# Performance work log

Measured on AMD Instinct MI355X. Metric: run time of the kernel, lower is better.

Reference implementation:

```python
import jax, jax.numpy as jnp
import numpy as np

N, E, H, K = 2000, 512, 8, 32
DH = E // H  # 64
CLAMP = 10000.0
LN_EPS = 1e-5


def _layernorm(x, g, b):
    mu = jnp.mean(x, axis=-1, keepdims=True)
    var = jnp.mean((x - mu) ** 2, axis=-1, keepdims=True)
    return (x - mu) * jax.lax.rsqrt(var + LN_EPS) * g + b


def setup_inputs() -> dict:
    key = jax.random.key(0)
    ks = jax.random.split(key, 16)
    s_in = 1.0 / np.sqrt(E)
    inp = {
        'x': jax.random.normal(ks[0], (N, E), jnp.float32),
        'coords9': jax.random.normal(ks[1], (N, 9), jnp.float32),
        'prompt_signal': jax.random.normal(ks[2], (E,), jnp.float32),
        # pos_encoder: Linear(3, E//4) + GELU + LayerNorm(E//4)
        'pos_w1': jax.random.normal(ks[3], (E // 4, 3), jnp.float32) * 0.5,
        'pos_b1': jax.random.normal(ks[4], (E // 4,), jnp.float32) * 0.02,
        'pos_ln_g': jnp.ones((E // 4,), jnp.float32),
        'pos_ln_b': jnp.zeros((E // 4,), jnp.float32),
        # MultiheadAttention in/out projections
        'wq': jax.random.normal(ks[5], (E, E), jnp.float32) * s_in,
        'wk': jax.random.normal(ks[6], (E, E), jnp.float32) * s_in,
        'wv': jax.random.normal(ks[7], (E, E), jnp.float32) * s_in,
        'bq': jnp.zeros((E,), jnp.float32),
        'bk': jnp.zeros((E,), jnp.float32),
        'bv': jnp.zeros((E,), jnp.float32),
        'wo': jax.random.normal(ks[8], (E, E), jnp.float32) * s_in,
        'bo': jnp.zeros((E,), jnp.float32),
    }
    return inp


def reference(x, coords9, prompt_signal, pos_w1, pos_b1, pos_ln_g, pos_ln_b,
              wq, wk, wv, bq, bk, bv, wo, bo):
    n = x.shape[0]
    # centroids of triangle faces: (N,3)
    centroids = coords9.reshape(n, 3, 3).mean(axis=1)
    # pairwise centroid distances (only relation feature that affects output)
    diff = centroids[:, None, :] - centroids[None, :, :]        # (N,N,3)
    distances = jnp.linalg.norm(diff, axis=-1)                   # (N,N)
    # positional encoding branch
    pos_enc = _layernorm(jax.nn.gelu(centroids @ pos_w1.T + pos_b1, approximate=False),
                         pos_ln_g, pos_ln_b)                     # (N,E/4)
    prompt_enhanced = x + prompt_signal[None, :]
    pos_enhanced = jnp.concatenate([prompt_enhanced[:, :3 * E // 4], pos_enc], axis=-1)  # (N,E)
    # top-k nearest neighbors mask (k smallest distances per row)
    _, topk_idx = jax.lax.top_k(-distances, K)                   # (N,K)
    attn_mask = jnp.full((n, n), -jnp.inf, jnp.float32)
    attn_mask = attn_mask.at[jnp.arange(n)[:, None], topk_idx].set(0.0)
    # multi-head attention, self q=k=v, fp32
    q = (pos_enhanced @ wq.T + bq).reshape(n, H, DH)
    k = (pos_enhanced @ wk.T + bk).reshape(n, H, DH)
    v = (pos_enhanced @ wv.T + bv).reshape(n, H, DH)
    scores = jnp.einsum('nhd,mhd->hnm', q, k) / np.sqrt(DH) + attn_mask[None]
    attn = jax.nn.softmax(scores, axis=-1)                       # (H,N,N)
    ctx = jnp.einsum('hnm,mhd->nhd', attn, v).reshape(n, E)
    out = ctx @ wo.T + bo
    # _sanitize_tensor
    out = jnp.nan_to_num(out, nan=0.0, posinf=CLAMP, neginf=-CLAMP)
    return jnp.clip(out, -CLAMP, CLAMP)
```

## Files before the change

kernel.cpp:

```cpp
#include <hip/hip_runtime.h>
#include <math.h>

#define NN_K 32
#define E_DIM 512
#define CLAMP_V 10000.0f

typedef __attribute__((ext_vector_type(8))) short short8;
typedef __attribute__((ext_vector_type(4))) float f32x4;

__device__ __forceinline__ unsigned short f2bf(float x) {
  unsigned u = __float_as_uint(x);
  unsigned r = u + 0x7fffu + ((u >> 16) & 1u);
  return (unsigned short)(r >> 16);
}
__device__ __forceinline__ float bf2f_bits(short h) {
  return __uint_as_float(((unsigned)(unsigned short)h) << 16);
}

__device__ __forceinline__ void async16(const void* g, void* l) {
  __builtin_amdgcn_global_load_lds((const __attribute__((address_space(1))) void*)g,
                                   (__attribute__((address_space(3))) void*)l, 16, 0, 0);
}

__global__ __launch_bounds__(256) void wconv_kernel(
    const float* __restrict__ wq, const float* __restrict__ wk,
    const float* __restrict__ wv, const float* __restrict__ wo,
    short* __restrict__ w_bf)
{
  int v = blockIdx.x * 256 + threadIdx.x;
  int m = v >> 16;
  int e = v & 0xffff;
  const float* src = m == 0 ? wq : (m == 1 ? wk : (m == 2 ? wv : wo));
  float4 f = ((const float4*)src)[e];
  short4 h;
  h.x = (short)f2bf(f.x); h.y = (short)f2bf(f.y);
  h.z = (short)f2bf(f.z); h.w = (short)f2bf(f.w);
  ((short4*)w_bf)[v] = h;
}

__global__ __launch_bounds__(128) void pos_kernel(
    const float* __restrict__ x, const float* __restrict__ coords9,
    const float* __restrict__ prompt,
    const float* __restrict__ w1, const float* __restrict__ b1,
    const float* __restrict__ ln_g, const float* __restrict__ ln_b,
    short* __restrict__ pos_bf, float* __restrict__ cent, int N)
{
  int n = blockIdx.x;
  int t = threadIdx.x;
  size_t rb = (size_t)n * E_DIM;
  if (n >= N) {
    #pragma unroll
    for (int j = t; j < E_DIM; j += 128) pos_bf[rb + j] = 0;
    return;
  }
  const float* c9 = coords9 + n * 9;
  float c0 = (c9[0] + c9[3] + c9[6]) / 3.0f;
  float c1 = (c9[1] + c9[4] + c9[7]) / 3.0f;
  float c2 = (c9[2] + c9[5] + c9[8]) / 3.0f;
  if (t == 0) { cent[n*3+0] = c0; cent[n*3+1] = c1; cent[n*3+2] = c2; }

  float pre = c0 * w1[t*3+0] + c1 * w1[t*3+1] + c2 * w1[t*3+2] + b1[t];
  float g = 0.5f * pre * (1.0f + erff(pre * 0.70710678118654752440f));

  __shared__ float red[4];
  float s = g;
  #pragma unroll
  for (int o = 32; o > 0; o >>= 1) s += __shfl_xor(s, o);
  if ((t & 63) == 0) red[t >> 6] = s;
  __syncthreads();
  float mu = (red[0] + red[1]) * (1.0f / 128.0f);
  float d = g - mu;
  float s2 = d * d;
  #pragma unroll
  for (int o = 32; o > 0; o >>= 1) s2 += __shfl_xor(s2, o);
  if ((t & 63) == 0) red[2 + (t >> 6)] = s2;
  __syncthreads();
  float var = (red[2] + red[3]) * (1.0f / 128.0f);
  float y = d * rsqrtf(var + 1e-5f) * ln_g[t] + ln_b[t];

  pos_bf[rb + 384 + t] = (short)f2bf(y);
  #pragma unroll
  for (int j = t; j < 384; j += 128)
    pos_bf[rb + j] = (short)f2bf(x[rb + j] + prompt[j]);
}

__global__ __launch_bounds__(256) void topk_kernel(
    const float* __restrict__ cent, int* __restrict__ topk, int N)
{
  __shared__ unsigned hist[256];
  __shared__ unsigned waveSums[4];
  __shared__ unsigned sel_bin, sel_rem;
  __shared__ unsigned cnt, tcnt;
  __shared__ unsigned tie[2048];

  int n = blockIdx.x;
  int t = threadIdx.x;
  int lane = t & 63, wid = t >> 6;
  float cx = cent[n*3+0], cy = cent[n*3+1], cz = cent[n*3+2];

  unsigned bits[8];
  #pragma unroll
  for (int r = 0; r < 8; ++r) {
    int m = t + (r << 8);
    unsigned b = 0xFFFFFFFFu;
    if (m < N) {
      float dx = cx - cent[m*3+0];
      float dy = cy - cent[m*3+1];
      float dz = cz - cent[m*3+2];
      float dist = sqrtf(dx*dx + dy*dy + dz*dz);
      b = __float_as_uint(dist);
    }
    bits[r] = b;
  }

  unsigned prefix = 0;
  unsigned K_rem = NN_K;
  #pragma unroll
  for (int p = 0; p < 4; ++p) {
    int shift = 24 - 8 * p;
    unsigned high_mask = (p == 0) ? 0u : (0xFFFFFFFFu << (8 * (4 - p)));
    hist[t] = 0;
    __syncthreads();
    #pragma unroll
    for (int r = 0; r < 8; ++r) {
      if ((bits[r] & high_mask) == prefix)
        atomicAdd(&hist[(bits[r] >> shift) & 255], 1u);
    }
    __syncthreads();
    unsigned h = hist[t];
    unsigned scan = h;
    #pragma unroll
    for (int o = 1; o < 64; o <<= 1) {
      unsigned u = __shfl_up(scan, o);
      if (lane >= o) scan += u;
    }
    if (lane == 63) waveSums[wid] = scan;
    __syncthreads();
    unsigned off = 0;
    for (int w = 0; w < wid; ++w) off += waveSums[w];
    scan += off;
    if (scan >= K_rem && (scan - h) < K_rem) {
      sel_bin = (unsigned)t;
      sel_rem = K_rem - (scan - h);
    }
    __syncthreads();
    prefix |= sel_bin << shift;
    K_rem = sel_rem;
    __syncthreads();
  }

  unsigned T = prefix;
  if (t == 0) { cnt = 0; tcnt = 0; }
  __syncthreads();
  #pragma unroll
  for (int r = 0; r < 8; ++r) {
    int m = t + (r << 8);
    if (m < N) {
      if (bits[r] < T) {
        unsigned slot = atomicAdd(&cnt, 1u);
        topk[n * NN_K + slot] = m;
      } else if (bits[r] == T) {
        unsigned tp = atomicAdd(&tcnt, 1u);
        tie[tp] = (unsigned)m;
      }
    }
  }
  __syncthreads();
  if (t == 0) {
    unsigned base = cnt;
    unsigned need = K_rem;
    for (unsigned it = 0; it < need; ++it) {
      unsigned best = 0xFFFFFFFFu, bj = 0;
      for (unsigned j = 0; j < tcnt; ++j)
        if (tie[j] < best) { best = tie[j]; bj = j; }
      topk[n * NN_K + base + it] = (int)best;
      tie[bj] = 0xFFFFFFFFu;
    }
  }
}

__device__ __forceinline__ void gemm_core(
    const short* __restrict__ A, const short* __restrict__ W,
    const float* __restrict__ bias,
    float* __restrict__ outf, short* __restrict__ outb,
    int out_ld, int out_c0,
    int M, int row0, int col0, bool doClamp)
{
  __shared__ short sA[2][4096], sB[2][4096];
  int tid = threadIdx.x;
  int cr = tid >> 2;
  int ck = (tid & 3) << 3;
  const short* gA = A + (size_t)(row0 + cr) * 512 + ck;
  const short* gB = W + (size_t)(col0 + cr) * 512 + ck;
  int lo0 = tid * 8, lo1 = (tid + 256) * 8;
  const size_t rstep = (size_t)64 * 512;

  int lane = tid & 63, wv_ = tid >> 6;
  int wm = (wv_ & 1) << 6, wn = (wv_ >> 1) << 6;
  int lr = lane & 15, lq = lane >> 4;

#define STAGE(t, b) do { \
    async16(gA + (t) * 32,         &sA[b][lo0]); \
    async16(gA + (t) * 32 + rstep, &sA[b][lo1]); \
    async16(gB + (t) * 32,         &sB[b][lo0]); \
    async16(gB + (t) * 32 + rstep, &sB[b][lo1]); } while (0)

  STAGE(0, 0);
  STAGE(1, 1);

  f32x4 acc[4][4];
  #pragma unroll
  for (int i = 0; i < 4; ++i)
    #pragma unroll
    for (int j = 0; j < 4; ++j)
      acc[i][j] = (f32x4){0.f, 0.f, 0.f, 0.f};

  #pragma unroll
  for (int it = 0; it < 16; ++it) {
    int cur = it & 1;
    if (it == 15) asm volatile("s_waitcnt vmcnt(0)\ns_barrier" ::: "memory");
    else          asm volatile("s_waitcnt vmcnt(4)\ns_barrier" ::: "memory");

    short8 af[4], bf[4];
    #pragma unroll
    for (int i = 0; i < 4; ++i) {
      af[i] = *(const short8*)&sA[cur][(wm + (i << 4) + lr) * 32 + (lq << 3)];
      bf[i] = *(const short8*)&sB[cur][(wn + (i << 4) + lr) * 32 + (lq << 3)];
    }
    #pragma unroll
    for (int i = 0; i < 4; ++i)
      #pragma unroll
      for (int j = 0; j < 4; ++j)
        acc[i][j] = __builtin_amdgcn_mfma_f32_16x16x32_bf16(af[i], bf[j], acc[i][j], 0, 0, 0);

    asm volatile("s_waitcnt lgkmcnt(0)\ns_barrier" ::: "memory");
    if (it + 2 < 16) STAGE(it + 2, cur);
  }
#undef STAGE

  #pragma unroll
  for (int j = 0; j < 4; ++j) {
    int gcol = col0 + wn + (j << 4) + lr;
    float bv_ = bias[gcol];
    #pragma unroll
    for (int i = 0; i < 4; ++i) {
      #pragma unroll
      for (int r = 0; r < 4; ++r) {
        int grow = row0 + wm + (i << 4) + (lq << 2) + r;
        if (grow < M) {
          float v = acc[i][j][r] + bv_;
          if (doClamp) {
            v = isnan(v) ? 0.0f : v;
            v = fminf(fmaxf(v, -CLAMP_V), CLAMP_V);
          }
          if (outf) outf[(size_t)grow * 512 + gcol] = v;
          else      outb[(size_t)grow * out_ld + out_c0 + gcol] = (short)f2bf(v);
        }
      }
    }
  }
}

__global__ __launch_bounds__(256) void qkv_mfma(
    const short* __restrict__ A, const short* __restrict__ Wb,
    const float* __restrict__ bq, const float* __restrict__ bk, const float* __restrict__ bv,
    float* __restrict__ qb, short* __restrict__ kv, int M)
{
  int sel = blockIdx.y >> 2;
  int nblk = blockIdx.y & 3;
  int r0 = blockIdx.x * 128, c0 = nblk * 128;
  if (sel == 0)
    gemm_core(A, Wb, bq, qb, nullptr, 512, 0, M, r0, c0, false);
  else if (sel == 1)
    gemm_core(A, Wb + 262144, bk, nullptr, kv, 1024, 0, M, r0, c0, false);
  else
    gemm_core(A, Wb + 2 * 262144, bv, nullptr, kv, 1024, 512, M, r0, c0, false);
}

__global__ __launch_bounds__(256) void out_mfma(
    const short* __restrict__ A, const short* __restrict__ Wb,
    const float* __restrict__ bias, float* __restrict__ out, int M)
{
  gemm_core(A, Wb + (size_t)3 * 262144, bias, out, nullptr, 512, 0, M,
            blockIdx.x * 128, blockIdx.y * 128, true);
}

__global__ __launch_bounds__(512) void attn_kernel(
    const float* __restrict__ qb, const short* __restrict__ kv,
    const int* __restrict__ topk, short* __restrict__ ctx_bf, int N)
{
  __shared__ short klds[32 * 512];
  __shared__ int sidx[NN_K];
  __shared__ float plds[8 * 32];

  int n = blockIdx.x;
  int tid = threadIdx.x;
  size_t rb = (size_t)n * E_DIM;
  if (n >= N) { ctx_bf[rb + tid] = 0; return; }

  if (tid < NN_K) sidx[tid] = topk[n * NN_K + tid];
  __syncthreads();

  int h = tid >> 6, lane = tid & 63;
  int jk = lane & 31, half = lane >> 5;
  int dbase = h * 64 + half * 32;

  float qv[32];
  {
    const float4* qs = (const float4*)(qb + rb + dbase);
    #pragma unroll
    for (int b = 0; b < 8; ++b) {
      float4 f = qs[b];
      qv[b*4+0] = f.x; qv[b*4+1] = f.y; qv[b*4+2] = f.z; qv[b*4+3] = f.w;
    }
  }

  {
    int j = tid >> 4, a = tid & 15;
    const short8* src = (const short8*)(kv + (size_t)sidx[j] * 1024 + a * 32);
    int sw = 4 * (j & 15);
    short* row = &klds[j * 512];
    #pragma unroll
    for (int b = 0; b < 4; ++b) {
      short8 val = src[b];
      int d0 = a * 32 + b * 8;
      *(short4*)&row[(d0    ) ^ sw] = *(const short4*)&val;
      *(short4*)&row[(d0 + 4) ^ sw] = *((const short4*)&val + 1);
    }
  }
  __syncthreads();

  float s = 0.f;
  {
    int sw = 4 * (jk & 15);
    const short* krow = &klds[jk * 512];
    #pragma unroll
    for (int i = 0; i < 32; ++i) {
      int d = (dbase + i) ^ sw;
      s += qv[i] * bf2f_bits(krow[d]);
    }
  }
  s += __shfl_xor(s, 32);
  s *= 0.125f;

  float mx = s;
  #pragma unroll
  for (int o = 16; o > 0; o >>= 1) mx = fmaxf(mx, __shfl_xor(mx, o));
  float p = expf(s - mx);
  float l = p;
  #pragma unroll
  for (int o = 16; o > 0; o >>= 1) l += __shfl_xor(l, o);
  p *= (1.0f / l);
  if (half == 0) plds[h * 32 + jk] = p;
  __syncthreads();

  float pv[32];
  #pragma unroll
  for (int b = 0; b < 8; ++b) {
    float4 f = *(const float4*)&plds[h * 32 + b * 4];
    pv[b*4+0] = f.x; pv[b*4+1] = f.y; pv[b*4+2] = f.z; pv[b*4+3] = f.w;
  }

  int off = 512 + h * 64 + lane;
  float acc = 0.f;
  #pragma unroll
  for (int j = 0; j < NN_K; ++j) {
    int ij = topk[n * NN_K + j];
    acc += pv[j] * bf2f_bits(kv[(size_t)ij * 1024 + off]);
  }
  ctx_bf[rb + h * 64 + lane] = (short)f2bf(acc);
}

extern "C" void kernel_launch(void* const* d_in, const int* in_sizes, int n_in,
                              void* d_out, int out_size, void* d_ws, size_t ws_size,
                              hipStream_t stream) {
  const float* x       = (const float*)d_in[0];
  const float* coords9 = (const float*)d_in[1];
  const float* prompt  = (const float*)d_in[2];
  const float* pos_w1  = (const float*)d_in[3];
  const float* pos_b1  = (const float*)d_in[4];
  const float* ln_g    = (const float*)d_in[5];
  const float* ln_b    = (const float*)d_in[6];
  const float* wq      = (const float*)d_in[7];
  const float* wk      = (const float*)d_in[8];
  const float* wv      = (const float*)d_in[9];
  const float* bq      = (const float*)d_in[10];
  const float* bk      = (const float*)d_in[11];
  const float* bv      = (const float*)d_in[12];
  const float* wo      = (const float*)d_in[13];
  const float* bo      = (const float*)d_in[14];

  int N = in_sizes[1] / 9;
  int Mpad = (N + 127) & ~127;
  size_t PE = (size_t)Mpad * E_DIM;

  char* p = (char*)d_ws;
  short* pos_bf = (short*)p; p += PE * 2;
  short* w_bf   = (short*)p; p += (size_t)4 * 512 * 512 * 2;
  float* qb     = (float*)p; p += PE * 4;
  short* kv_bf  = (short*)p; p += PE * 2 * 2;
  short* ctx_bf = (short*)p; p += PE * 2;
  float* cent   = (float*)p; p += (size_t)N * 3 * 4;
  int*   topk   = (int*)p;

  wconv_kernel<<<1024, 256, 0, stream>>>(wq, wk, wv, wo, w_bf);
  pos_kernel<<<Mpad, 128, 0, stream>>>(x, coords9, prompt, pos_w1, pos_b1,
                                       ln_g, ln_b, pos_bf, cent, N);
  topk_kernel<<<N, 256, 0, stream>>>(cent, topk, N);

  dim3 gq(Mpad / 128, 12);
  qkv_mfma<<<gq, 256, 0, stream>>>(pos_bf, w_bf, bq, bk, bv, qb, kv_bf, Mpad);
  attn_kernel<<<Mpad, 512, 0, stream>>>(qb, kv_bf, topk, ctx_bf, N);

  dim3 go(Mpad / 128, 4);
  out_mfma<<<go, 256, 0, stream>>>(ctx_bf, w_bf, bo, (float*)d_out, N);
}
```

Baseline: 168.0 us.

## Fuse weight conversion, pos-encoding and top-k into one kernel; shrink GEMM tiles

Merges the weight bf16 conversion, positional-encoding and top-k kernels into a single front kernel, dispatched by block index, to remove two launches and the centroid buffer. Centroids are now recomputed from coords9 inside the top-k path. The shared GEMM core moves from 128x128 to 64x128 tiles so the QKV and output projections launch twice as many blocks, which should fill more CUs but lowers per-block reuse. The attention kernel also reads K rows with short4 loads and takes neighbour indices from shared memory instead of reloading them from global memory. The front kernel's branch boundary is hardcoded to 2304 blocks, which only matches Mpad = 2048.

```diff
diff --git a/kernel.cpp b/kernel.cpp
--- a/kernel.cpp
+++ b/kernel.cpp
@@ -22,159 +22,172 @@
                                    (__attribute__((address_space(3))) void*)l, 16, 0, 0);
 }
 
-__global__ __launch_bounds__(256) void wconv_kernel(
-    const float* __restrict__ wq, const float* __restrict__ wk,
-    const float* __restrict__ wv, const float* __restrict__ wo,
-    short* __restrict__ w_bf)
-{
-  int v = blockIdx.x * 256 + threadIdx.x;
-  int m = v >> 16;
-  int e = v & 0xffff;
-  const float* src = m == 0 ? wq : (m == 1 ? wk : (m == 2 ? wv : wo));
-  float4 f = ((const float4*)src)[e];
-  short4 h;
-  h.x = (short)f2bf(f.x); h.y = (short)f2bf(f.y);
-  h.z = (short)f2bf(f.z); h.w = (short)f2bf(f.w);
-  ((short4*)w_bf)[v] = h;
-}
-
-__global__ __launch_bounds__(128) void pos_kernel(
+__global__ __launch_bounds__(256) void front_kernel(
     const float* __restrict__ x, const float* __restrict__ coords9,
     const float* __restrict__ prompt,
     const float* __restrict__ w1, const float* __restrict__ b1,
     const float* __restrict__ ln_g, const float* __restrict__ ln_b,
-    short* __restrict__ pos_bf, float* __restrict__ cent, int N)
+    const float* __restrict__ wq, const float* __restrict__ wk,
+    const float* __restrict__ wv, const float* __restrict__ wo,
+    short* __restrict__ w_bf, short* __restrict__ pos_bf,
+    int* __restrict__ topk, int N, int Mpad)
 {
-  int n = blockIdx.x;
+  int blk = blockIdx.x;
   int t = threadIdx.x;
-  size_t rb = (size_t)n * E_DIM;
-  if (n >= N) {
-    #pragma unroll
-    for (int j = t; j < E_DIM; j += 128) pos_bf[rb + j] = 0;
+
+  if (blk < 256) {
+    #pragma unroll
+    for (int i = 0; i < 4; ++i) {
+      int v = blk * 256 + t + i * 65536;
+      int m = v >> 16;
+      int e = v & 0xffff;
+      const float* src = m == 0 ? wq : (m == 1 ? wk : (m == 2 ? wv : wo));
+      float4 f = ((const float4*)src)[e];
+      short4 h;
+      h.x = (short)f2bf(f.x); h.y = (short)f2bf(f.y);
+      h.z = (short)f2bf(f.z); h.w = (short)f2bf(f.w);
+      ((short4*)w_bf)[v] = h;
+    }
     return;
   }
-  const float* c9 = coords9 + n * 9;
-  float c0 = (c9[0] + c9[3] + c9[6]) / 3.0f;
-  float c1 = (c9[1] + c9[4] + c9[7]) / 3.0f;
-  float c2 = (c9[2] + c9[5] + c9[8]) / 3.0f;
-  if (t == 0) { cent[n*3+0] = c0; cent[n*3+1] = c1; cent[n*3+2] = c2; }
-
-  float pre = c0 * w1[t*3+0] + c1 * w1[t*3+1] + c2 * w1[t*3+2] + b1[t];
-  float g = 0.5f * pre * (1.0f + erff(pre * 0.70710678118654752440f));
-
-  __shared__ float red[4];
-  float s = g;
-  #pragma unroll
-  for (int o = 32; o > 0; o >>= 1) s += __shfl_xor(s, o);
-  if ((t & 63) == 0) red[t >> 6] = s;
-  __syncthreads();
-  float mu = (red[0] + red[1]) * (1.0f / 128.0f);
-  float d = g - mu;
-  float s2 = d * d;
-  #pragma unroll
-  for (int o = 32; o > 0; o >>= 1) s2 += __shfl_xor(s2, o);
-  if ((t & 63) == 0) red[2 + (t >> 6)] = s2;
-  __syncthreads();
-  float var = (red[2] + red[3]) * (1.0f / 128.0f);
-  float y = d * rsqrtf(var + 1e-5f) * ln_g[t] + ln_b[t];
-
-  pos_bf[rb + 384 + t] = (short)f2bf(y);
-  #pragma unroll
-  for (int j = t; j < 384; j += 128)
-    pos_bf[rb + j] = (short)f2bf(x[rb + j] + prompt[j]);
-}
-
-__global__ __launch_bounds__(256) void topk_kernel(
-    const float* __restrict__ cent, int* __restrict__ topk, int N)
-{
-  __shared__ unsigned hist[256];
-  __shared__ unsigned waveSums[4];
-  __shared__ unsigned sel_bin, sel_rem;
-  __shared__ unsigned cnt, tcnt;
-  __shared__ unsigned tie[2048];
-
-  int n = blockIdx.x;
-  int t = threadIdx.x;
-  int lane = t & 63, wid = t >> 6;
-  float cx = cent[n*3+0], cy = cent[n*3+1], cz = cent[n*3+2];
-
-  unsigned bits[8];
-  #pragma unroll
-  for (int r = 0; r < 8; ++r) {
-    int m = t + (r << 8);
-    unsigned b = 0xFFFFFFFFu;
-    if (m < N) {
-      float dx = cx - cent[m*3+0];
-      float dy = cy - cent[m*3+1];
-      float dz = cz - cent[m*3+2];
-      float dist = sqrtf(dx*dx + dy*dy + dz*dz);
-      b = __float_as_uint(dist);
-    }
-    bits[r] = b;
-  }
-
-  unsigned prefix = 0;
-  unsigned K_rem = NN_K;
-  #pragma unroll
-  for (int p = 0; p < 4; ++p) {
-    int shift = 24 - 8 * p;
-    unsigned high_mask = (p == 0) ? 0u : (0xFFFFFFFFu << (8 * (4 - p)));
-    hist[t] = 0;
+
+  if (blk < 2304) {
+    int n = blk - 256;
+    size_t rb = (size_t)n * E_DIM;
+    if (n >= N) {
+      #pragma unroll
+      for (int j = t; j < E_DIM; j += 256) pos_bf[rb + j] = 0;
+      return;
+    }
+    __shared__ float red[4];
+    float g = 0.f;
+    if (t < 128) {
+      const float* c9 = coords9 + n * 9;
+      float c0 = (c9[0] + c9[3] + c9[6]) / 3.0f;
+      float c1 = (c9[1] + c9[4] + c9[7]) / 3.0f;
+      float c2 = (c9[2] + c9[5] + c9[8]) / 3.0f;
+      float pre = c0 * w1[t*3+0] + c1 * w1[t*3+1] + c2 * w1[t*3+2] + b1[t];
+      g = 0.5f * pre * (1.0f + erff(pre * 0.70710678118654752440f));
+      float s = g;
+      #pragma unroll
+      for (int o = 32; o > 0; o >>= 1) s += __shfl_xor(s, o);
+      if ((t & 63) == 0) red[t >> 6] = s;
+    }
     __syncthreads();
+    float mu = (red[0] + red[1]) * (1.0f / 128.0f);
+    float d = g - mu;
+    if (t < 128) {
+      float s2 = d * d;
+      #pragma unroll
+      for (int o = 32; o > 0; o >>= 1) s2 += __shfl_xor(s2, o);
+      if ((t & 63) == 0) red[2 + (t >> 6)] = s2;
+    }
+    __syncthreads();
+    if (t < 128) {
+      float var = (red[2] + red[3]) * (1.0f / 128.0f);
+      float y = d * rsqrtf(var + 1e-5f) * ln_g[t] + ln_b[t];
+      pos_bf[rb + 384 + t] = (short)f2bf(y);
+    }
+    #pragma unroll
+    for (int j = t; j < 384; j += 256)
+      pos_bf[rb + j] = (short)f2bf(x[rb + j] + prompt[j]);
+    return;
+  }
+
+  {
+    __shared__ unsigned hist[256];
+    __shared__ unsigned waveSums[4];
+    __shared__ unsigned sel_bin, sel_rem;
+    __shared__ unsigned cnt, tcnt;
+    __shared__ unsigned tie[2048];
+
+    int n = blk - 2304;
+    int lane = t & 63, wid = t >> 6;
+    const float* cn = coords9 + n * 9;
+    float cx = (cn[0] + cn[3] + cn[6]) / 3.0f;
+    float cy = (cn[1] + cn[4] + cn[7]) / 3.0f;
+    float cz = (cn[2] + cn[5] + cn[8]) / 3.0f;
+
+    unsigned bits[8];
     #pragma unroll
     for (int r = 0; r < 8; ++r) {
-      if ((bits[r] & high_mask) == prefix)
-        atomicAdd(&hist[(bits[r] >> shift) & 255], 1u);
-    }
+      int m = t + (r << 8);
+      unsigned b = 0xFFFFFFFFu;
+      if (m < N) {
+        const float* cm = coords9 + m * 9;
+        float mx_ = (cm[0] + cm[3] + cm[6]) / 3.0f;
+        float my_ = (cm[1] + cm[4] + cm[7]) / 3.0f;
+        float mz_ = (cm[2] + cm[5] + cm[8]) / 3.0f;
+        float dx = cx - mx_, dy = cy - my_, dz = cz - mz_;
+        float dist = sqrtf(dx*dx + dy*dy + dz*dz);
+        b = __float_as_uint(dist);
+      }
+      bits[r] = b;
+    }
+
+    unsigned prefix = 0;
+    unsigned K_rem = NN_K;
+    #pragma unroll
+    for (int p = 0; p < 4; ++p) {
+      int shift = 24 - 8 * p;
+      unsigned high_mask = (p == 0) ? 0u : (0xFFFFFFFFu << (8 * (4 - p)));
+      hist[t] = 0;
+      __syncthreads();
+      #pragma unroll
+      for (int r = 0; r < 8; ++r) {
+        if ((bits[r] & high_mask) == prefix)
+          atomicAdd(&hist[(bits[r] >> shift) & 255], 1u);
+      }
+      __syncthreads();
+      unsigned h = hist[t];
+      unsigned scan = h;
+      #pragma unroll
+      for (int o = 1; o < 64; o <<= 1) {
+        unsigned u = __shfl_up(scan, o);
+        if (lane >= o) scan += u;
+      }
+      if (lane == 63) waveSums[wid] = scan;
+      __syncthreads();
+      unsigned off = 0;
+      for (int w = 0; w < wid; ++w) off += waveSums[w];
+      scan += off;
+      if (scan >= K_rem && (scan - h) < K_rem) {
+        sel_bin = (unsigned)t;
+        sel_rem = K_rem - (scan - h);
+      }
+      __syncthreads();
+      prefix |= sel_bin << shift;
+      K_rem = sel_rem;
+      __syncthreads();
+    }
+
+    unsigned T = prefix;
+    if (t == 0) { cnt = 0; tcnt = 0; }
     __syncthreads();
-    unsigned h = hist[t];
-    unsigned scan = h;
-    #pragma unroll
-    for (int o = 1; o < 64; o <<= 1) {
-      unsigned u = __shfl_up(scan, o);
-      if (lane >= o) scan += u;
-    }
-    if (lane == 63) waveSums[wid] = scan;
+    #pragma unroll
+    for (int r = 0; r < 8; ++r) {
+      int m = t + (r << 8);
+      if (m < N) {
+        if (bits[r] < T) {
+          unsigned slot = atomicAdd(&cnt, 1u);
+          topk[n * NN_K + slot] = m;
+        } else if (bits[r] == T) {
+          unsigned tp = atomicAdd(&tcnt, 1u);
+          tie[tp] = (unsigned)m;
+        }
+      }
+    }
     __syncthreads();
-    unsigned off = 0;
-    for (int w = 0; w < wid; ++w) off += waveSums[w];
-    scan += off;
-    if (scan >= K_rem && (scan - h) < K_rem) {
-      sel_bin = (unsigned)t;
-      sel_rem = K_rem - (scan - h);
-    }
-    __syncthreads();
-    prefix |= sel_bin << shift;
-    K_rem = sel_rem;
-    __syncthreads();
-  }
-
-  unsigned T = prefix;
-  if (t == 0) { cnt = 0; tcnt = 0; }
-  __syncthreads();
-  #pragma unroll
-  for (int r = 0; r < 8; ++r) {
-    int m = t + (r << 8);
-    if (m < N) {
-      if (bits[r] < T) {
-        unsigned slot = atomicAdd(&cnt, 1u);
-        topk[n * NN_K + slot] = m;
-      } else if (bits[r] == T) {
-        unsigned tp = atomicAdd(&tcnt, 1u);
-        tie[tp] = (unsigned)m;
-      }
-    }
-  }
-  __syncthreads();
-  if (t == 0) {
-    unsigned base = cnt;
-    unsigned need = K_rem;
-    for (unsigned it = 0; it < need; ++it) {
-      unsigned best = 0xFFFFFFFFu, bj = 0;
-      for (unsigned j = 0; j < tcnt; ++j)
-        if (tie[j] < best) { best = tie[j]; bj = j; }
-      topk[n * NN_K + base + it] = (int)best;
-      tie[bj] = 0xFFFFFFFFu;
+    if (t == 0) {
+      unsigned base = cnt;
+      unsigned need = K_rem;
+      for (unsigned it = 0; it < need; ++it) {
+        unsigned best = 0xFFFFFFFFu, bj = 0;
+        for (unsigned j = 0; j < tcnt; ++j)
+          if (tie[j] < best) { best = tie[j]; bj = j; }
+        topk[n * NN_K + base + it] = (int)best;
+        tie[bj] = 0xFFFFFFFFu;
+      }
     }
   }
 }
@@ -186,51 +199,51 @@
     int out_ld, int out_c0,
     int M, int row0, int col0, bool doClamp)
 {
-  __shared__ short sA[2][4096], sB[2][4096];
+  __shared__ short sA[2][64 * 32], sB[2][128 * 32];
   int tid = threadIdx.x;
   int cr = tid >> 2;
   int ck = (tid & 3) << 3;
   const short* gA = A + (size_t)(row0 + cr) * 512 + ck;
   const short* gB = W + (size_t)(col0 + cr) * 512 + ck;
-  int lo0 = tid * 8, lo1 = (tid + 256) * 8;
+  int lo = tid * 8, loB1 = (tid + 256) * 8;
   const size_t rstep = (size_t)64 * 512;
 
   int lane = tid & 63, wv_ = tid >> 6;
-  int wm = (wv_ & 1) << 6, wn = (wv_ >> 1) << 6;
+  int wn = wv_ << 5;
   int lr = lane & 15, lq = lane >> 4;
 
 #define STAGE(t, b) do { \
-    async16(gA + (t) * 32,         &sA[b][lo0]); \
-    async16(gA + (t) * 32 + rstep, &sA[b][lo1]); \
-    async16(gB + (t) * 32,         &sB[b][lo0]); \
-    async16(gB + (t) * 32 + rstep, &sB[b][lo1]); } while (0)
+    async16(gA + (t) * 32,         &sA[b][lo]); \
+    async16(gB + (t) * 32,         &sB[b][lo]); \
+    async16(gB + (t) * 32 + rstep, &sB[b][loB1]); } while (0)
 
   STAGE(0, 0);
   STAGE(1, 1);
 
-  f32x4 acc[4][4];
+  f32x4 acc[4][2];
   #pragma unroll
   for (int i = 0; i < 4; ++i)
     #pragma unroll
-    for (int j = 0; j < 4; ++j)
+    for (int j = 0; j < 2; ++j)
       acc[i][j] = (f32x4){0.f, 0.f, 0.f, 0.f};
 
   #pragma unroll
   for (int it = 0; it < 16; ++it) {
     int cur = it & 1;
     if (it == 15) asm volatile("s_waitcnt vmcnt(0)\ns_barrier" ::: "memory");
-    else          asm volatile("s_waitcnt vmcnt(4)\ns_barrier" ::: "memory");
-
-    short8 af[4], bf[4];
-    #pragma unroll
-    for (int i = 0; i < 4; ++i) {
-      af[i] = *(const short8*)&sA[cur][(wm + (i << 4) + lr) * 32 + (lq << 3)];
-      bf[i] = *(const short8*)&sB[cur][(wn + (i << 4) + lr) * 32 + (lq << 3)];
-    }
+    else          asm volatile("s_waitcnt vmcnt(3)\ns_barrier" ::: "memory");
+
+    short8 af[4], bf[2];
     #pragma unroll
     for (int i = 0; i < 4; ++i)
-      #pragma unroll
-      for (int j = 0; j < 4; ++j)
+      af[i] = *(const short8*)&sA[cur][((i << 4) + lr) * 32 + (lq << 3)];
+    #pragma unroll
+    for (int j = 0; j < 2; ++j)
+      bf[j] = *(const short8*)&sB[cur][(wn + (j << 4) + lr) * 32 + (lq << 3)];
+    #pragma unroll
+    for (int i = 0; i < 4; ++i)
+      #pragma unroll
+      for (int j = 0; j < 2; ++j)
         acc[i][j] = __builtin_amdgcn_mfma_f32_16x16x32_bf16(af[i], bf[j], acc[i][j], 0, 0, 0);
 
     asm volatile("s_waitcnt lgkmcnt(0)\ns_barrier" ::: "memory");
@@ -239,14 +252,14 @@
 #undef STAGE
 
   #pragma unroll
-  for (int j = 0; j < 4; ++j) {
+  for (int j = 0; j < 2; ++j) {
     int gcol = col0 + wn + (j << 4) + lr;
     float bv_ = bias[gcol];
     #pragma unroll
     for (int i = 0; i < 4; ++i) {
       #pragma unroll
       for (int r = 0; r < 4; ++r) {
-        int grow = row0 + wm + (i << 4) + (lq << 2) + r;
+        int grow = row0 + (i << 4) + (lq << 2) + r;
         if (grow < M) {
           float v = acc[i][j][r] + bv_;
           if (doClamp) {
@@ -268,7 +281,7 @@
 {
   int sel = blockIdx.y >> 2;
   int nblk = blockIdx.y & 3;
-  int r0 = blockIdx.x * 128, c0 = nblk * 128;
+  int r0 = blockIdx.x * 64, c0 = nblk * 128;
   if (sel == 0)
     gemm_core(A, Wb, bq, qb, nullptr, 512, 0, M, r0, c0, false);
   else if (sel == 1)
@@ -282,7 +295,7 @@
     const float* __restrict__ bias, float* __restrict__ out, int M)
 {
   gemm_core(A, Wb + (size_t)3 * 262144, bias, out, nullptr, 512, 0, M,
-            blockIdx.x * 128, blockIdx.y * 128, true);
+            blockIdx.x * 64, blockIdx.y * 128, true);
 }
 
 __global__ __launch_bounds__(512) void attn_kernel(
@@ -335,9 +348,10 @@
     int sw = 4 * (jk & 15);
     const short* krow = &klds[jk * 512];
     #pragma unroll
-    for (int i = 0; i < 32; ++i) {
-      int d = (dbase + i) ^ sw;
-      s += qv[i] * bf2f_bits(krow[d]);
+    for (int i4 = 0; i4 < 8; ++i4) {
+      short4 kkv = *(const short4*)&krow[(dbase + i4 * 4) ^ sw];
+      s += qv[i4*4+0] * bf2f_bits(kkv.x) + qv[i4*4+1] * bf2f_bits(kkv.y)
+         + qv[i4*4+2] * bf2f_bits(kkv.z) + qv[i4*4+3] * bf2f_bits(kkv.w);
     }
   }
   s += __shfl_xor(s, 32);
@@ -364,10 +378,8 @@
   int off = 512 + h * 64 + lane;
   float acc = 0.f;
   #pragma unroll
-  for (int j = 0; j < NN_K; ++j) {
-    int ij = topk[n * NN_K + j];
-    acc += pv[j] * bf2f_bits(kv[(size_t)ij * 1024 + off]);
-  }
+  for (int j = 0; j < NN_K; ++j)
+    acc += pv[j] * bf2f_bits(kv[(size_t)sidx[j] * 1024 + off]);
   ctx_bf[rb + h * 64 + lane] = (short)f2bf(acc);
 }
 
@@ -400,18 +412,16 @@
   float* qb     = (float*)p; p += PE * 4;
   short* kv_bf  = (short*)p; p += PE * 2 * 2;
   short* ctx_bf = (short*)p; p += PE * 2;
-  float* cent   = (float*)p; p += (size_t)N * 3 * 4;
   int*   topk   = (int*)p;
 
-  wconv_kernel<<<1024, 256, 0, stream>>>(wq, wk, wv, wo, w_bf);
-  pos_kernel<<<Mpad, 128, 0, stream>>>(x, coords9, prompt, pos_w1, pos_b1,
-                                       ln_g, ln_b, pos_bf, cent, N);
-  topk_kernel<<<N, 256, 0, stream>>>(cent, topk, N);
-
-  dim3 gq(Mpad / 128, 12);
+  front_kernel<<<256 + Mpad + N, 256, 0, stream>>>(
+      x, coords9, prompt, pos_w1, pos_b1, ln_g, ln_b,
+      wq, wk, wv, wo, w_bf, pos_bf, topk, N, Mpad);
+
+  dim3 gq(Mpad / 64, 12);
   qkv_mfma<<<gq, 256, 0, stream>>>(pos_bf, w_bf, bq, bk, bv, qb, kv_bf, Mpad);
   attn_kernel<<<Mpad, 512, 0, stream>>>(qb, kv_bf, topk, ctx_bf, N);
 
-  dim3 go(Mpad / 128, 4);
+  dim3 go(Mpad / 64, 4);
   out_mfma<<<go, 256, 0, stream>>>(ctx_bf, w_bf, bo, (float*)d_out, N);
 }
```

Result: faster. 152.9 us (-9.0%).
